# Optimization experiments

Measured on AMD Instinct MI355X. Metric: run time of the kernel, lower is better.

Reference implementation:

```python
import jax, jax.numpy as jnp
import numpy as np
import math

B, N, F = 16, 1024, 1024
OUT = 1024

def setup_inputs() -> dict:
    key = jax.random.key(0)
    k1, k2, k3, k4 = jax.random.split(key, 4)
    prott5_emd = jax.random.normal(k1, (B, N, F), dtype=jnp.float32)
    # shared (dense) normalized adjacency, as the original applies one adj to every sample
    adj = jax.random.uniform(k2, (N, N), dtype=jnp.float32)
    adj = adj / jnp.sum(adj, axis=1, keepdims=True)  # row-normalize like a GCN propagation matrix
    h0 = jax.random.normal(k3, (B, N, F), dtype=jnp.float32)
    stdv = 1.0 / math.sqrt(OUT)
    weight = jax.random.uniform(k4, (F, OUT), minval=-stdv, maxval=stdv, dtype=jnp.float32)
    return {"prott5_emd": prott5_emd, "adj": adj, "h0": h0, "weight": weight,
            "lamda": 0.5, "alpha": 0.1, "l": 1}

def reference(prott5_emd, adj, h0, weight, lamda, alpha, l):
    # GraphConvolution (GCNII-style), variant=False, residual=False
    theta = min(1.0, math.log(lamda / l + 1.0))  # static python scalar
    # batched aggregation: adj @ x_i for every sample i  ->  [B, N, F]
    hi = jnp.einsum('nm,bmf->bnf', adj, prott5_emd)
    support = (1.0 - alpha) * hi + alpha * h0          # affine combine with initial features
    out = theta * jnp.einsum('bnf,fo->bno', support, weight) + (1.0 - theta) * support
    return out
```

## Files before the change

### kernel.cpp

```cpp
#include <hip/hip_runtime.h>
#include <hip/hip_bf16.h>

typedef __attribute__((ext_vector_type(8))) short bf16x8;
typedef __attribute__((ext_vector_type(4))) float f32x4;
typedef __attribute__((ext_vector_type(4))) unsigned int u32x4;
typedef __attribute__((ext_vector_type(2))) unsigned int u32x2;

__device__ __forceinline__ float b2f(unsigned short u) {
  unsigned int x = ((unsigned int)u) << 16;
  float f;
  __builtin_memcpy(&f, &x, 4);
  return f;
}
__device__ __forceinline__ unsigned short f2b(float f) {
  __hip_bfloat16 h = __float2bfloat16(f);
  unsigned short u;
  __builtin_memcpy(&u, &h, 2);
  return u;
}
__device__ __forceinline__ float ldE(const float* p) { return *p; }
__device__ __forceinline__ float ldE(const unsigned short* p) { return b2f(*p); }
__device__ __forceinline__ void stC(float* p, float v) { *p = v; }
__device__ __forceinline__ void stC(unsigned short* p, float v) { *p = f2b(v); }

__global__ __launch_bounds__(256) void conv_transpose64(
    const float* __restrict__ src, unsigned short* __restrict__ dst,
    int R, int C) {
  __shared__ unsigned short tile[64][68];
  const int b = blockIdx.z;
  const float* s = src + (size_t)b * R * C;
  unsigned short* d = dst + (size_t)b * R * C;
  const int r0 = blockIdx.y * 64, c0 = blockIdx.x * 64;
  const int t = threadIdx.x;
#pragma unroll
  for (int p = 0; p < 4; ++p) {
    const int id = t + 256 * p;
    const int r = id >> 4, c4 = (id & 15) * 4;
    f32x4 v = *(const f32x4*)(s + (size_t)(r0 + r) * C + (c0 + c4));
#pragma unroll
    for (int j = 0; j < 4; ++j) tile[r][c4 + j] = f2b(v[j]);
  }
  __syncthreads();
#pragma unroll
  for (int p = 0; p < 2; ++p) {
    const int id = t + 256 * p;
    const int oc = id >> 3, cr8 = (id & 7) * 8;
    u32x4 v;
    unsigned short* pv = (unsigned short*)&v;
#pragma unroll
    for (int j = 0; j < 8; ++j) pv[j] = tile[cr8 + j][oc];
    *(u32x4*)(d + (size_t)(c0 + oc) * R + (r0 + cr8)) = v;
  }
}

__global__ __launch_bounds__(256) void conv_transpose_wprime(
    const float* __restrict__ src, unsigned short* __restrict__ dst,
    float scale, float diag) {
  __shared__ float tile[64][65];
  const int r0 = blockIdx.y * 64, c0 = blockIdx.x * 64;
  const int t = threadIdx.x;
#pragma unroll
  for (int p = 0; p < 4; ++p) {
    const int id = t + 256 * p;
    const int r = id >> 4, c4 = (id & 15) * 4;
    f32x4 v = *(const f32x4*)(src + (size_t)(r0 + r) * 1024 + (c0 + c4));
#pragma unroll
    for (int j = 0; j < 4; ++j) tile[r][c4 + j] = v[j];
  }
  __syncthreads();
#pragma unroll
  for (int p = 0; p < 2; ++p) {
    const int id = t + 256 * p;
    const int oc = id >> 3, cr8 = (id & 7) * 8;
    u32x4 v;
    unsigned short* pv = (unsigned short*)&v;
#pragma unroll
    for (int j = 0; j < 8; ++j) {
      const int o = c0 + oc, f = r0 + cr8 + j;
      float val = scale * tile[cr8 + j][oc] + (o == f ? diag : 0.f);
      pv[j] = f2b(val);
    }
    *(u32x4*)(dst + (size_t)(c0 + oc) * 1024 + (r0 + cr8)) = v;
  }
}

__global__ __launch_bounds__(256) void conv_bf16(const float* __restrict__ src,
                                                 unsigned short* __restrict__ dst,
                                                 int n) {
  const int i = (blockIdx.x * 256 + threadIdx.x) * 4;
  if (i >= n) return;
  f32x4 v = *(const f32x4*)(src + i);
  unsigned short o[4];
#pragma unroll
  for (int j = 0; j < 4; ++j) o[j] = f2b(v[j]);
  u32x2 pk;
  __builtin_memcpy(&pk, o, 8);
  *(u32x2*)(dst + i) = pk;
}

template <int DECOMP, typename ET, typename CT, bool HASE>
__global__ __launch_bounds__(512, 2) void gemm256(
    const unsigned short* __restrict__ A, const unsigned short* __restrict__ BT,
    const ET* __restrict__ E, CT* __restrict__ C, float c0, float c1) {
  constexpr int K = 1024;
  constexpr int NT = 16;
  constexpr size_t NF = 1024ull * 1024ull;
  __shared__ unsigned short lds[4][16384];
  const int bid = blockIdx.x;
  const int nid = (bid & 7) * 32 + (bid >> 3);
  int ty, tx;
  if (DECOMP == 0) { ty = nid >> 6; tx = nid & 63; }
  else             { ty = nid >> 2; tx = nid & 3; }
  const size_t m0 = (size_t)ty * 256, n0 = (size_t)tx * 256;

  const int t = threadIdx.x, lane = t & 63, wv = t >> 6;
  const int wm = (wv >> 2) * 128, wn = (wv & 3) * 64;

  f32x4 acc[8][4];
#pragma unroll
  for (int i = 0; i < 8; ++i)
#pragma unroll
    for (int j = 0; j < 4; ++j) acc[i][j] = (f32x4){0.f, 0.f, 0.f, 0.f};

  bf16x8 areg[4][2], b0r[2][2], b1r[2][2];

  auto STAGE = [&](int buf, int op, int half, const unsigned short* gbase,
                   size_t rowbase, int k0) {
#pragma unroll
    for (int l = 0; l < 2; ++l) {
      const int id = l * 512 + t;
      const int rl = id >> 3, c = id & 7;
      const int gc = (c ^ (rl & 7)) << 3;
      const unsigned short* g =
          gbase + (rowbase + half * 128 + rl) * K + k0 + gc;
      unsigned short* dst =
          &lds[buf * 2 + op][half * 8192 + (l * 512 + wv * 64) * 8];
      __builtin_amdgcn_global_load_lds(
          (const __attribute__((address_space(1))) unsigned int*)g,
          (__attribute__((address_space(3))) unsigned int*)dst, 16, 0, 0);
    }
  };

#define LOAD_A(MH)                                                     \
  {                                                                    \
    const unsigned short* Ard = lds[rd * 2 + 0];                       \
    _Pragma("unroll") for (int mi = 0; mi < 4; ++mi)                   \
        _Pragma("unroll") for (int kk = 0; kk < 2; ++kk) {             \
      const int row = wm + (MH)*64 + mi * 16 + (lane & 15);            \
      const int ch = ((kk * 4 + (lane >> 4)) ^ (row & 7)) << 3;        \
      areg[mi][kk] = *(const bf16x8*)(Ard + row * 64 + ch);            \
    }                                                                  \
  }
#define LOAD_B(NH, BR)                                                 \
  {                                                                    \
    const unsigned short* Brd = lds[rd * 2 + 1];                       \
    _Pragma("unroll") for (int nj = 0; nj < 2; ++nj)                   \
        _Pragma("unroll") for (int kk = 0; kk < 2; ++kk) {             \
      const int row = wn + (NH)*32 + nj * 16 + (lane & 15);            \
      const int ch = ((kk * 4 + (lane >> 4)) ^ (row & 7)) << 3;        \
      BR[nj][kk] = *(const bf16x8*)(Brd + row * 64 + ch);              \
    }                                                                  \
  }
#define MFMA_Q(MH, NH, BR)                                             \
  do {                                                                 \
    __builtin_amdgcn_s_setprio(1);                                     \
    _Pragma("unroll") for (int mi = 0; mi < 4; ++mi)                   \
        _Pragma("unroll") for (int nj = 0; nj < 2; ++nj)               \
            _Pragma("unroll") for (int kk = 0; kk < 2; ++kk)           \
        acc[(MH)*4 + mi][(NH)*2 + nj] =                                \
        __builtin_amdgcn_mfma_f32_16x16x32_bf16(                       \
            areg[mi][kk], BR[nj][kk], acc[(MH)*4 + mi][(NH)*2 + nj],   \
            0, 0, 0);                                                  \
    __builtin_amdgcn_s_setprio(0);                                     \
  } while (0)
#define LGKM0                                          \
  asm volatile("s_waitcnt lgkmcnt(0)" ::: "memory");   \
  __builtin_amdgcn_sched_barrier(0)

  STAGE(0, 0, 0, A, m0, 0);
  STAGE(0, 0, 1, A, m0, 0);
  STAGE(0, 1, 0, BT, n0, 0);
  STAGE(0, 1, 1, BT, n0, 0);
  STAGE(1, 1, 0, BT, n0, 64);
  STAGE(1, 0, 0, A, m0, 64);
  asm volatile("s_waitcnt vmcnt(4)" ::: "memory");
  __builtin_amdgcn_s_barrier();

  for (int tt = 0; tt < NT; ++tt) {
    const int rd = tt & 1;
    LOAD_A(0);
    LOAD_B(0, b0r);
    if (tt + 1 < NT) STAGE((tt + 1) & 1, 1, 1, BT, n0, (tt + 1) * 64);
    __builtin_amdgcn_s_barrier();
    LGKM0;
    MFMA_Q(0, 0, b0r);
    __builtin_amdgcn_s_barrier();
    LOAD_B(1, b1r);
    if (tt + 1 < NT) STAGE((tt + 1) & 1, 0, 1, A, m0, (tt + 1) * 64);
    __builtin_amdgcn_s_barrier();
    LGKM0;
    MFMA_Q(0, 1, b1r);
    __builtin_amdgcn_s_barrier();
    LOAD_A(1);
    if (tt + 2 < NT) STAGE(rd, 1, 0, BT, n0, (tt + 2) * 64);
    __builtin_amdgcn_s_barrier();
    LGKM0;
    MFMA_Q(1, 1, b1r);
    __builtin_amdgcn_s_barrier();
    if (tt + 2 < NT) STAGE(rd, 0, 0, A, m0, (tt + 2) * 64);
    __builtin_amdgcn_s_barrier();
    LGKM0;
    MFMA_Q(1, 0, b0r);
    asm volatile("s_waitcnt vmcnt(4)" ::: "memory");
    __builtin_amdgcn_s_barrier();
  }

  size_t base;
  if (DECOMP == 0)
    base = (n0 >> 10) * NF + (n0 & 1023) + m0 * 1024;
  else
    base = m0 * 1024 + n0;
  const ET* Eb = E + base;
  CT* Cb = C + base;
#pragma unroll
  for (int mi = 0; mi < 8; ++mi) {
#pragma unroll
    for (int r = 0; r < 4; ++r) {
      const int lrow = wm + mi * 16 + (lane >> 4) * 4 + r;
#pragma unroll
      for (int nj = 0; nj < 4; ++nj) {
        const int lcol = wn + nj * 16 + (lane & 15);
        float v = c0 * acc[mi][nj][r];
        if (HASE) v += c1 * ldE(Eb + (size_t)lrow * 1024 + lcol);
        stC(Cb + (size_t)lrow * 1024 + lcol, v);
      }
    }
  }
#undef LOAD_A
#undef LOAD_B
#undef MFMA_Q
#undef LGKM0
}

extern "C" void kernel_launch(void* const* d_in, const int* in_sizes, int n_in,
                              void* d_out, int out_size, void* d_ws,
                              size_t ws_size, hipStream_t stream) {
  const float* X = (const float*)d_in[0];
  const float* adj = (const float*)d_in[1];
  const float* h0 = (const float*)d_in[2];
  const float* W = (const float*)d_in[3];
  float* out = (float*)d_out;

  const size_t NF = 1024ull * 1024ull;
  unsigned short* XT = (unsigned short*)d_ws;
  unsigned short* WT = XT + 16 * NF;
  unsigned short* AJ = WT + NF;
  unsigned short* S = AJ + NF;

  const float theta = 0.405465108f;
  const float alpha = 0.1f;

  conv_transpose64<<<dim3(16, 16, 16), 256, 0, stream>>>(X, XT, 1024, 1024);
  conv_transpose_wprime<<<dim3(16, 16, 1), 256, 0, stream>>>(
      W, WT, theta, 1.0f - theta);
  conv_bf16<<<dim3(1024), 256, 0, stream>>>(adj, AJ, 1024 * 1024);

  gemm256<0, float, unsigned short, true>
      <<<dim3(256), 512, 0, stream>>>(AJ, XT, h0, S, 1.0f - alpha, alpha);
  gemm256<1, unsigned short, float, false>
      <<<dim3(256), 512, 0, stream>>>(S, WT, (const unsigned short*)S, out,
                                      1.0f, 0.0f);
}
```

Before: 114.7 us.

## Fuse h0 residual add into second GEMM's A-operand staging

The alpha*h0 term is no longer added in the first GEMM epilogue, where each thread issued scattered scalar fp32 loads of h0. The second GEMM now loads h0 tiles into an LDS scratch buffer with async global-to-LDS copies, adds them to the bf16 S tile in registers, and writes the combined bf16 operand into swizzled LDS inside the pipelined K loop. This removes the uncoalesced h0 reads from the first GEMM's epilogue. In exchange it adds 32KB of LDS, extra barriers and conversion work in the second GEMM's main loop, which may reduce occupancy or MFMA overlap.

```diff
diff --git a/kernel.cpp b/kernel.cpp
--- a/kernel.cpp
+++ b/kernel.cpp
@@ -18,10 +18,6 @@
   __builtin_memcpy(&u, &h, 2);
   return u;
 }
-__device__ __forceinline__ float ldE(const float* p) { return *p; }
-__device__ __forceinline__ float ldE(const unsigned short* p) { return b2f(*p); }
-__device__ __forceinline__ void stC(float* p, float v) { *p = v; }
-__device__ __forceinline__ void stC(unsigned short* p, float v) { *p = f2b(v); }
 
 __global__ __launch_bounds__(256) void conv_transpose64(
     const float* __restrict__ src, unsigned short* __restrict__ dst,
@@ -98,48 +94,22 @@
   *(u32x2*)(dst + i) = pk;
 }
 
-template <int DECOMP, typename ET, typename CT, bool HASE>
-__global__ __launch_bounds__(512, 2) void gemm256(
-    const unsigned short* __restrict__ A, const unsigned short* __restrict__ BT,
-    const ET* __restrict__ E, CT* __restrict__ C, float c0, float c1) {
-  constexpr int K = 1024;
-  constexpr int NT = 16;
-  constexpr size_t NF = 1024ull * 1024ull;
-  __shared__ unsigned short lds[4][16384];
-  const int bid = blockIdx.x;
-  const int nid = (bid & 7) * 32 + (bid >> 3);
-  int ty, tx;
-  if (DECOMP == 0) { ty = nid >> 6; tx = nid & 63; }
-  else             { ty = nid >> 2; tx = nid & 3; }
-  const size_t m0 = (size_t)ty * 256, n0 = (size_t)tx * 256;
-
-  const int t = threadIdx.x, lane = t & 63, wv = t >> 6;
-  const int wm = (wv >> 2) * 128, wn = (wv & 3) * 64;
-
-  f32x4 acc[8][4];
-#pragma unroll
-  for (int i = 0; i < 8; ++i)
-#pragma unroll
-    for (int j = 0; j < 4; ++j) acc[i][j] = (f32x4){0.f, 0.f, 0.f, 0.f};
-
-  bf16x8 areg[4][2], b0r[2][2], b1r[2][2];
-
-  auto STAGE = [&](int buf, int op, int half, const unsigned short* gbase,
-                   size_t rowbase, int k0) {
-#pragma unroll
-    for (int l = 0; l < 2; ++l) {
-      const int id = l * 512 + t;
-      const int rl = id >> 3, c = id & 7;
-      const int gc = (c ^ (rl & 7)) << 3;
-      const unsigned short* g =
-          gbase + (rowbase + half * 128 + rl) * K + k0 + gc;
-      unsigned short* dst =
-          &lds[buf * 2 + op][half * 8192 + (l * 512 + wv * 64) * 8];
-      __builtin_amdgcn_global_load_lds(
-          (const __attribute__((address_space(1))) unsigned int*)g,
-          (__attribute__((address_space(3))) unsigned int*)dst, 16, 0, 0);
-    }
-  };
+__device__ __forceinline__ void stage_tile16(unsigned short* ldsbase,
+                                             const unsigned short* __restrict__ gbase,
+                                             size_t rowbase, int half, int k0,
+                                             int t, int wv) {
+#pragma unroll
+  for (int l = 0; l < 2; ++l) {
+    const int id = l * 512 + t;
+    const int rl = id >> 3, c = id & 7;
+    const int gc = (c ^ (rl & 7)) << 3;
+    const unsigned short* g = gbase + (rowbase + half * 128 + rl) * 1024 + k0 + gc;
+    unsigned short* dst = ldsbase + half * 8192 + (l * 512 + wv * 64) * 8;
+    __builtin_amdgcn_global_load_lds(
+        (const __attribute__((address_space(1))) unsigned int*)g,
+        (__attribute__((address_space(3))) unsigned int*)dst, 16, 0, 0);
+  }
+}
 
 #define LOAD_A(MH)                                                     \
   {                                                                    \
@@ -176,52 +146,57 @@
 #define LGKM0                                          \
   asm volatile("s_waitcnt lgkmcnt(0)" ::: "memory");   \
   __builtin_amdgcn_sched_barrier(0)
-
-  STAGE(0, 0, 0, A, m0, 0);
-  STAGE(0, 0, 1, A, m0, 0);
-  STAGE(0, 1, 0, BT, n0, 0);
-  STAGE(0, 1, 1, BT, n0, 0);
-  STAGE(1, 1, 0, BT, n0, 64);
-  STAGE(1, 0, 0, A, m0, 64);
+#define BAR __builtin_amdgcn_s_barrier()
+#define MEMFENCE asm volatile("" ::: "memory")
+
+__global__ __launch_bounds__(512, 2) void gemm1(
+    const unsigned short* __restrict__ A, const unsigned short* __restrict__ BT,
+    unsigned short* __restrict__ Cq, float c0) {
+  constexpr int NT = 16;
+  constexpr size_t NF = 1024ull * 1024ull;
+  __shared__ unsigned short lds[4][16384];
+  const int bid = blockIdx.x;
+  const int nid = (bid & 7) * 32 + (bid >> 3);
+  const size_t m0 = (size_t)(nid >> 6) * 256, n0 = (size_t)(nid & 63) * 256;
+  const int t = threadIdx.x, lane = t & 63, wv = t >> 6;
+  const int wm = (wv >> 2) * 128, wn = (wv & 3) * 64;
+
+  f32x4 acc[8][4];
+#pragma unroll
+  for (int i = 0; i < 8; ++i)
+#pragma unroll
+    for (int j = 0; j < 4; ++j) acc[i][j] = (f32x4){0.f, 0.f, 0.f, 0.f};
+  bf16x8 areg[4][2], b0r[2][2], b1r[2][2];
+
+  stage_tile16(lds[0], A, m0, 0, 0, t, wv);
+  stage_tile16(lds[0], A, m0, 1, 0, t, wv);
+  stage_tile16(lds[1], BT, n0, 0, 0, t, wv);
+  stage_tile16(lds[1], BT, n0, 1, 0, t, wv);
+  stage_tile16(lds[3], BT, n0, 0, 64, t, wv);
+  stage_tile16(lds[2], A, m0, 0, 64, t, wv);
   asm volatile("s_waitcnt vmcnt(4)" ::: "memory");
-  __builtin_amdgcn_s_barrier();
+  BAR;
 
   for (int tt = 0; tt < NT; ++tt) {
-    const int rd = tt & 1;
+    const int rd = tt & 1, wr = rd ^ 1;
     LOAD_A(0);
     LOAD_B(0, b0r);
-    if (tt + 1 < NT) STAGE((tt + 1) & 1, 1, 1, BT, n0, (tt + 1) * 64);
-    __builtin_amdgcn_s_barrier();
-    LGKM0;
-    MFMA_Q(0, 0, b0r);
-    __builtin_amdgcn_s_barrier();
+    if (tt + 1 < NT) stage_tile16(lds[wr * 2 + 1], BT, n0, 1, (tt + 1) * 64, t, wv);
+    BAR; LGKM0; MFMA_Q(0, 0, b0r); BAR;
     LOAD_B(1, b1r);
-    if (tt + 1 < NT) STAGE((tt + 1) & 1, 0, 1, A, m0, (tt + 1) * 64);
-    __builtin_amdgcn_s_barrier();
-    LGKM0;
-    MFMA_Q(0, 1, b1r);
-    __builtin_amdgcn_s_barrier();
+    if (tt + 1 < NT) stage_tile16(lds[wr * 2 + 0], A, m0, 1, (tt + 1) * 64, t, wv);
+    BAR; LGKM0; MFMA_Q(0, 1, b1r); BAR;
     LOAD_A(1);
-    if (tt + 2 < NT) STAGE(rd, 1, 0, BT, n0, (tt + 2) * 64);
-    __builtin_amdgcn_s_barrier();
-    LGKM0;
-    MFMA_Q(1, 1, b1r);
-    __builtin_amdgcn_s_barrier();
-    if (tt + 2 < NT) STAGE(rd, 0, 0, A, m0, (tt + 2) * 64);
-    __builtin_amdgcn_s_barrier();
-    LGKM0;
-    MFMA_Q(1, 0, b0r);
+    if (tt + 2 < NT) stage_tile16(lds[rd * 2 + 1], BT, n0, 0, (tt + 2) * 64, t, wv);
+    BAR; LGKM0; MFMA_Q(1, 1, b1r); BAR;
+    if (tt + 2 < NT) stage_tile16(lds[rd * 2 + 0], A, m0, 0, (tt + 2) * 64, t, wv);
+    BAR; LGKM0; MFMA_Q(1, 0, b0r);
     asm volatile("s_waitcnt vmcnt(4)" ::: "memory");
-    __builtin_amdgcn_s_barrier();
-  }
-
-  size_t base;
-  if (DECOMP == 0)
-    base = (n0 >> 10) * NF + (n0 & 1023) + m0 * 1024;
-  else
-    base = m0 * 1024 + n0;
-  const ET* Eb = E + base;
-  CT* Cb = C + base;
+    BAR;
+  }
+
+  const size_t base = (n0 >> 10) * NF + (n0 & 1023) + m0 * 1024;
+  unsigned short* Cb = Cq + base;
 #pragma unroll
   for (int mi = 0; mi < 8; ++mi) {
 #pragma unroll
@@ -230,17 +205,149 @@
 #pragma unroll
       for (int nj = 0; nj < 4; ++nj) {
         const int lcol = wn + nj * 16 + (lane & 15);
-        float v = c0 * acc[mi][nj][r];
-        if (HASE) v += c1 * ldE(Eb + (size_t)lrow * 1024 + lcol);
-        stC(Cb + (size_t)lrow * 1024 + lcol, v);
+        Cb[(size_t)lrow * 1024 + lcol] = f2b(c0 * acc[mi][nj][r]);
       }
     }
   }
+}
+
+#define G2_LOAD_S(SR, H, K0)                                                  \
+  {                                                                           \
+    _Pragma("unroll") for (int l = 0; l < 2; ++l) {                           \
+      const int id = l * 512 + t, rl = id >> 3, cc = id & 7;                  \
+      SR[l] = *(const u32x4*)(Sp + (m0 + (H)*128 + rl) * 1024 + (K0) + cc * 8); \
+    }                                                                         \
+  }
+#define G2_GL_SCR(H, K0)                                                      \
+  {                                                                           \
+    _Pragma("unroll") for (int l2 = 0; l2 < 4; ++l2) {                        \
+      const int id2 = l2 * 512 + t;                                           \
+      const float* g = Hp + (m0 + (H)*128 + (id2 >> 4)) * 1024 + (K0) +       \
+                       (id2 & 15) * 4;                                        \
+      __builtin_amdgcn_global_load_lds(                                       \
+          (const __attribute__((address_space(1))) unsigned int*)g,           \
+          (__attribute__((address_space(3))) unsigned int*)(scr + l2 * 2048 + \
+                                                            wv * 256),        \
+          16, 0, 0);                                                          \
+    }                                                                         \
+  }
+#define G2_CVT_WRITE(H, WB, SR)                                               \
+  {                                                                           \
+    _Pragma("unroll") for (int l = 0; l < 2; ++l) {                           \
+      const int id = l * 512 + t, rl = id >> 3, cc = id & 7;                  \
+      const f32x4 ha = *(const f32x4*)(scr + id * 8);                         \
+      const f32x4 hb = *(const f32x4*)(scr + id * 8 + 4);                     \
+      const u32x4 sv = SR[l];                                                 \
+      u32x4 ov;                                                               \
+      _Pragma("unroll") for (int w = 0; w < 4; ++w) {                         \
+        const float hlo = (w < 2) ? ha[2 * w] : hb[2 * w - 4];                \
+        const float hhi = (w < 2) ? ha[2 * w + 1] : hb[2 * w - 3];            \
+        const float r0 = b2f((unsigned short)(sv[w] & 0xffffu)) + 0.1f * hlo; \
+        const float r1 = b2f((unsigned short)(sv[w] >> 16)) + 0.1f * hhi;     \
+        ov[w] = (unsigned int)f2b(r0) | ((unsigned int)f2b(r1) << 16);        \
+      }                                                                       \
+      *(u32x4*)(&lds[(WB)*2 + 0][(H)*8192 + rl * 64 + ((cc ^ (rl & 7)) << 3)]) = ov; \
+    }                                                                         \
+  }
+
+__global__ __launch_bounds__(512, 2) void gemm2(
+    const unsigned short* __restrict__ Sp, const unsigned short* __restrict__ BT,
+    const float* __restrict__ Hp, float* __restrict__ Co) {
+  constexpr int NT = 16;
+  __shared__ unsigned short lds[4][16384];
+  __shared__ float scr[8192];
+  const int bid = blockIdx.x;
+  const int nid = (bid & 7) * 32 + (bid >> 3);
+  const size_t m0 = (size_t)(nid >> 2) * 256, n0 = (size_t)(nid & 3) * 256;
+  const int t = threadIdx.x, lane = t & 63, wv = t >> 6;
+  const int wm = (wv >> 2) * 128, wn = (wv & 3) * 64;
+
+  f32x4 acc[8][4];
+#pragma unroll
+  for (int i = 0; i < 8; ++i)
+#pragma unroll
+    for (int j = 0; j < 4; ++j) acc[i][j] = (f32x4){0.f, 0.f, 0.f, 0.f};
+  bf16x8 areg[4][2], b0r[2][2], b1r[2][2];
+  u32x4 s0[2], s1[2];
+
+  G2_GL_SCR(0, 0);
+  G2_LOAD_S(s0, 0, 0);
+  asm volatile("s_waitcnt vmcnt(0)" ::: "memory");
+  BAR;
+  G2_CVT_WRITE(0, 0, s0);
+  BAR;
+  G2_GL_SCR(1, 0);
+  G2_LOAD_S(s1, 1, 0);
+  asm volatile("s_waitcnt vmcnt(0)" ::: "memory");
+  BAR;
+  G2_CVT_WRITE(1, 0, s1);
+  stage_tile16(lds[1], BT, n0, 0, 0, t, wv);
+  stage_tile16(lds[1], BT, n0, 1, 0, t, wv);
+  MEMFENCE;
+  stage_tile16(lds[3], BT, n0, 0, 64, t, wv);
+  asm volatile("s_waitcnt vmcnt(2) lgkmcnt(0)" ::: "memory");
+  BAR;
+
+  for (int tt = 0; tt < NT; ++tt) {
+    const int rd = tt & 1, wr = rd ^ 1;
+    const int k1 = (tt + 1) * 64;
+    const bool hasA = (tt + 1 < NT);
+    LOAD_A(0);
+    LOAD_B(0, b0r);
+    if (hasA) {
+      G2_GL_SCR(0, k1);
+      G2_LOAD_S(s0, 0, k1);
+      stage_tile16(lds[wr * 2 + 1], BT, n0, 1, k1, t, wv);
+    }
+    BAR; LGKM0; MFMA_Q(0, 0, b0r); BAR;
+    LOAD_B(1, b1r);
+    if (hasA) G2_LOAD_S(s1, 1, k1);
+    BAR; LGKM0; MFMA_Q(0, 1, b1r);
+    asm volatile("s_waitcnt vmcnt(2)" ::: "memory");
+    BAR;
+    LOAD_A(1);
+    if (hasA) G2_CVT_WRITE(0, wr, s0);
+    BAR; LGKM0;
+    if (hasA) {
+      G2_GL_SCR(1, k1);
+      MEMFENCE;
+    }
+    if (tt + 2 < NT) stage_tile16(lds[rd * 2 + 1], BT, n0, 0, (tt + 2) * 64, t, wv);
+    MFMA_Q(1, 1, b1r);
+    if (tt + 2 < NT) {
+      asm volatile("s_waitcnt vmcnt(2)" ::: "memory");
+    } else {
+      asm volatile("s_waitcnt vmcnt(0)" ::: "memory");
+    }
+    BAR;
+    if (hasA) G2_CVT_WRITE(1, wr, s1);
+    BAR; LGKM0; MFMA_Q(1, 0, b0r); BAR;
+  }
+
+  float* Cb = Co + m0 * 1024 + n0;
+#pragma unroll
+  for (int mi = 0; mi < 8; ++mi) {
+#pragma unroll
+    for (int r = 0; r < 4; ++r) {
+      const int lrow = wm + mi * 16 + (lane >> 4) * 4 + r;
+#pragma unroll
+      for (int nj = 0; nj < 4; ++nj) {
+        const int lcol = wn + nj * 16 + (lane & 15);
+        Cb[(size_t)lrow * 1024 + lcol] = acc[mi][nj][r];
+      }
+    }
+  }
+}
+
 #undef LOAD_A
 #undef LOAD_B
 #undef MFMA_Q
 #undef LGKM0
-}
+#undef BAR
+#undef MEMFENCE
+#undef G2_LOAD_S
+#undef G2_GL_SCR
+#undef G2_CVT_WRITE
 
 extern "C" void kernel_launch(void* const* d_in, const int* in_sizes, int n_in,
                               void* d_out, int out_size, void* d_ws,
@@ -258,16 +365,12 @@
   unsigned short* S = AJ + NF;
 
   const float theta = 0.405465108f;
-  const float alpha = 0.1f;
 
   conv_transpose64<<<dim3(16, 16, 16), 256, 0, stream>>>(X, XT, 1024, 1024);
   conv_transpose_wprime<<<dim3(16, 16, 1), 256, 0, stream>>>(
       W, WT, theta, 1.0f - theta);
   conv_bf16<<<dim3(1024), 256, 0, stream>>>(adj, AJ, 1024 * 1024);
 
-  gemm256<0, float, unsigned short, true>
-      <<<dim3(256), 512, 0, stream>>>(AJ, XT, h0, S, 1.0f - alpha, alpha);
-  gemm256<1, unsigned short, float, false>
-      <<<dim3(256), 512, 0, stream>>>(S, WT, (const unsigned short*)S, out,
-                                      1.0f, 0.0f);
-}
+  gemm1<<<dim3(256), 512, 0, stream>>>(AJ, XT, S, 0.9f);
+  gemm2<<<dim3(256), 512, 0, stream>>>(S, WT, h0, out);
+}
```

New measurement: 163.9 us. 42.9% more time.
